# Kernel optimization log

Hardware: AMD Instinct MI355X
Metric: run time of the kernel (lower is better)

The kernel has to match this reference:

```python
import math
import jax, jax.numpy as jnp
import numpy as np

B, N, D, H = 8, 512, 1024, 16
HD = D // H
K_DEFAULT, K_MAX, PROX_THR = 8, 12, 20.0


def setup_inputs() -> dict:
    key = jax.random.key(0)
    ks = jax.random.split(key, 12)
    tokens_B = jax.random.normal(ks[0], (B, N, D), dtype=jnp.float32)
    ego_distances = jax.random.uniform(ks[1], (B, N), dtype=jnp.float32)
    ego_mask = jnp.zeros((B, N), dtype=bool).at[:, 0].set(True)  # token 0 is ego
    ego_speed = jax.random.uniform(ks[2], (B,), dtype=jnp.float32)
    s = 1.0 / math.sqrt(D)
    Wq = jax.random.normal(ks[3], (D, D), jnp.float32) * s
    Wk = jax.random.normal(ks[4], (D, D), jnp.float32) * s
    Wv = jax.random.normal(ks[5], (D, D), jnp.float32) * s
    Weq = jax.random.normal(ks[6], (D, D), jnp.float32) * s
    Wo = jax.random.normal(ks[7], (D, D), jnp.float32) * (0.02 * s)
    Dm = D // 4
    W1 = jax.random.normal(ks[8], (Dm, 2), jnp.float32) * (1.0 / math.sqrt(2))
    b1 = jnp.zeros((Dm,), jnp.float32)
    W2 = jax.random.normal(ks[9], (H, Dm), jnp.float32) * (1.0 / math.sqrt(Dm))
    b2 = jnp.zeros((H,), jnp.float32)
    return dict(tokens_B=tokens_B, ego_distances=ego_distances, ego_mask=ego_mask,
                ego_speed=ego_speed, Wq=Wq, Wk=Wk, Wv=Wv, Weq=Weq, Wo=Wo,
                W1=W1, b1=b1, W2=W2, b2=b2)


def _compute_K(ego_speed, ego_distances):
    # deterministic, no-grad lookup (torch: @torch.no_grad)
    n = ego_distances.shape[1]
    close = (ego_distances < PROX_THR).astype(jnp.float32).sum(-1)
    density = close / max(n, 1)
    avg_speed = float(jnp.mean(ego_speed))
    avg_density = float(jnp.mean(density))
    K = K_DEFAULT
    if avg_speed > 15.0:
        K = min(K + 1, K_MAX)
    if avg_density > 0.5:
        K = min(K + 1, K_MAX)
    return min(K, n - 1)


def reference(tokens_B, ego_distances, ego_mask, ego_speed, Wq, Wk, Wv, Weq, Wo, W1, b1, W2, b2):
    b, n, d = tokens_B.shape
    K = _compute_K(ego_speed, ego_distances)
    if K <= 0:
        return jnp.zeros_like(tokens_B)

    # top-K nearest-to-ego neighbors per token, excluding self
    eye = jnp.eye(n, dtype=bool)
    dist_rank = jnp.where(eye[None, :, :], jnp.inf, ego_distances[:, None, :])  # (B,N,N)
    _, topk_idx = jax.lax.top_k(-dist_rank, K)  # (B,N,K) indices of smallest dists

    neighbors = jax.vmap(lambda t, idx: t[idx])(tokens_B, topk_idx)  # (B,N,K,D)

    is_ego = ego_mask.astype(tokens_B.dtype)[..., None]
    Q = (1.0 - is_ego) * (tokens_B @ Wq.T) + is_ego * (tokens_B @ Weq.T)
    Km = neighbors @ Wk.T
    Vm = neighbors @ Wv.T

    Q = Q.reshape(b, n, H, HD).transpose(0, 2, 1, 3)              # (B,H,N,hd)
    Km = Km.reshape(b, n, K, H, HD).transpose(0, 3, 1, 2, 4)      # (B,H,N,K,hd)
    Vm = Vm.reshape(b, n, K, H, HD).transpose(0, 3, 1, 2, 4)

    scores = jnp.einsum('bhnd,bhnkd->bhnk', Q, Km) / math.sqrt(HD)

    # additive pairwise distance bias MLP on (d_i_to_ego, d_j_to_ego)
    d_i = jnp.broadcast_to(ego_distances[:, :, None], (b, n, K))
    d_j = jax.vmap(lambda dd, idx: dd[idx])(ego_distances, topk_idx)
    dist_pair = jnp.stack([d_i, d_j], axis=-1)                    # (B,N,K,2)
    bias = jax.nn.relu(dist_pair @ W1.T + b1) @ W2.T + b2         # (B,N,K,H)
    scores = scores + bias.transpose(0, 3, 1, 2)                  # FIX-1: additive

    attn = jax.nn.softmax(scores, axis=-1)
    out = jnp.einsum('bhnk,bhnkd->bhnd', attn, Vm)
    out = out.transpose(0, 2, 1, 3).reshape(b, n, d)              # FIX-2 axis order
    return out @ Wo.T
```

## Files before the change

### kernel.cpp

```cpp
#include <hip/hip_runtime.h>
#include <math.h>

#define Bn 8
#define Nn 512
#define Dn 1024
#define Hn 16
#define HDn 64
#define KMAX 12
#define NSMAX 13
#define PROX 20.0f

typedef __attribute__((ext_vector_type(8))) short bf16x8;
typedef __attribute__((ext_vector_type(4))) float f32x4;

__device__ __forceinline__ unsigned short f2bf(float f) {
    unsigned int u = __float_as_uint(f);
    return (unsigned short)((u + 0x7FFFu + ((u >> 16) & 1u)) >> 16);
}

__global__ __launch_bounds__(256) void cvt_meta_kernel(const float* __restrict__ tokens,
                                                       const float* __restrict__ Wq,
                                                       const float* __restrict__ Wo,
                                                       const float* __restrict__ Wk,
                                                       const float* __restrict__ Wv,
                                                       const float* __restrict__ dist,
                                                       const float* __restrict__ speed,
                                                       unsigned short* __restrict__ tok_h,
                                                       unsigned short* __restrict__ wq_h,
                                                       unsigned short* __restrict__ wo_h,
                                                       unsigned short* __restrict__ wkv_h,
                                                       int* __restrict__ meta,
                                                       int* __restrict__ Lidx,
                                                       unsigned short* __restrict__ tok_g) {
    int blk = blockIdx.x;
    if (blk < 8192) {
        const float* src;
        unsigned short* dst;
        int local;
        if (blk < 4096) { src = tokens; dst = tok_h; local = blk; }
        else if (blk < 5120) { src = Wq; dst = wq_h; local = blk - 4096; }
        else if (blk < 6144) { src = Wo; dst = wo_h; local = blk - 5120; }
        else if (blk < 7168) { src = Wk; dst = wkv_h; local = blk - 6144; }
        else { src = Wv; dst = wkv_h + (size_t)Dn * Dn; local = blk - 7168; }
        int i = (local * 256 + threadIdx.x) * 4;
        float4 v = *(const float4*)&src[i];
        ushort4 o;
        o.x = f2bf(v.x); o.y = f2bf(v.y); o.z = f2bf(v.z); o.w = f2bf(v.w);
        *(ushort4*)&dst[i] = o;
        return;
    }
    if (threadIdx.x >= 64) return;
    int lane = threadIdx.x;
    int b = blk - 8192;

    int cnt = 0;
    for (int i = lane; i < Bn * Nn; i += 64) cnt += (dist[i] < PROX) ? 1 : 0;
    for (int off = 32; off; off >>= 1) cnt += __shfl_xor(cnt, off);

    float sp = 0.f;
    for (int i = lane; i < Bn; i += 64) sp += speed[i];
    for (int off = 32; off; off >>= 1) sp += __shfl_xor(sp, off);

    float avg_density = (float)cnt / (float)(Bn * Nn);
    float avg_speed = sp / (float)Bn;
    int K = 8;
    if (avg_speed > 15.0f) K = min(K + 1, KMAX);
    if (avg_density > 0.5f) K = min(K + 1, KMAX);
    K = min(K, Nn - 1);
    if (b == 0 && lane == 0) meta[0] = K;
    int ns = K + 1;

    int sel[NSMAX];
    float dloc[Nn / 64];
    #pragma unroll
    for (int j = 0; j < Nn / 64; ++j) dloc[j] = dist[b * Nn + lane + 64 * j];
    for (int r = 0; r < ns; ++r) {
        float mv = 1e30f;
        int mi = 0;
        #pragma unroll
        for (int j = 0; j < Nn / 64; ++j) {
            if (dloc[j] < mv) { mv = dloc[j]; mi = lane + 64 * j; }
        }
        for (int off = 32; off; off >>= 1) {
            float ov = __shfl_xor(mv, off);
            int oi = __shfl_xor(mi, off);
            if (ov < mv || (ov == mv && oi < mi)) { mv = ov; mi = oi; }
        }
        sel[r] = mi;
        if (lane == 0) Lidx[b * NSMAX + r] = mi;
        if ((mi & 63) == lane) dloc[mi >> 6] = 1e30f;
    }

    for (int s = 0; s < ns; ++s) {
        const float* src = &tokens[(size_t)(b * Nn + sel[s]) * Dn];
        unsigned short* dst = &tok_g[(size_t)(b * 16 + s) * Dn];
        #pragma unroll
        for (int q = 0; q < 4; ++q) {
            float4 v = *(const float4*)&src[(q * 64 + lane) * 4];
            ushort4 o;
            o.x = f2bf(v.x); o.y = f2bf(v.y); o.z = f2bf(v.z); o.w = f2bf(v.w);
            *(ushort4*)&dst[(q * 64 + lane) * 4] = o;
        }
    }
}

__device__ __forceinline__ void gemm_body_s(const unsigned short* A,
                                            const unsigned short* Bm,
                                            float* Cf, unsigned short* Ch,
                                            int Nd, int Kd, int sA, int sB,
                                            int bm, int bn, int mode, int hh,
                                            unsigned short* As, unsigned short* Bs) {
    int t = threadIdx.x;
    int wave = t >> 6, lane = t & 63;
    int wm = wave >> 1, wn = wave & 1;

    int srow = lane >> 2;
    int skoff = (lane & 3) * 8;
    const unsigned short* Ag  = A  + (size_t)(bm + wave * 16 + srow) * sA + skoff;
    const unsigned short* Bg  = Bm + (size_t)(bn + wave * 32 + srow) * sB + skoff;
    const unsigned short* Bg2 = Bg + (size_t)16 * sB;
    unsigned short* AsW  = As + (wave * 16) * 32;
    unsigned short* BsW  = Bs + (wave * 32) * 32;
    unsigned short* BsW2 = BsW + 16 * 32;

    f32x4 acc[2][4] = {};

    int fm = lane & 15;
    int fk = (lane >> 4) * 8;

    for (int k0 = 0; k0 < Kd; k0 += 32) {
        __builtin_amdgcn_global_load_lds((const __attribute__((address_space(1))) void*)Ag,
                                         (__attribute__((address_space(3))) void*)AsW, 16, 0, 0);
        __builtin_amdgcn_global_load_lds((const __attribute__((address_space(1))) void*)Bg,
                                         (__attribute__((address_space(3))) void*)BsW, 16, 0, 0);
        __builtin_amdgcn_global_load_lds((const __attribute__((address_space(1))) void*)Bg2,
                                         (__attribute__((address_space(3))) void*)BsW2, 16, 0, 0);
        Ag += 32; Bg += 32; Bg2 += 32;
        __syncthreads();

        bf16x8 af[2], bfr[4];
        #pragma unroll
        for (int mi = 0; mi < 2; ++mi)
            af[mi] = *(const bf16x8*)&As[(wm * 32 + mi * 16 + fm) * 32 + fk];
        #pragma unroll
        for (int ni = 0; ni < 4; ++ni)
            bfr[ni] = *(const bf16x8*)&Bs[(wn * 64 + ni * 16 + fm) * 32 + fk];
        #pragma unroll
        for (int mi = 0; mi < 2; ++mi)
            #pragma unroll
            for (int ni = 0; ni < 4; ++ni)
                acc[mi][ni] = __builtin_amdgcn_mfma_f32_16x16x32_bf16(af[mi], bfr[ni], acc[mi][ni], 0, 0, 0);
        __syncthreads();
    }

    int erow = (lane >> 4) * 4;
    #pragma unroll
    for (int mi = 0; mi < 2; ++mi)
        #pragma unroll
        for (int ni = 0; ni < 4; ++ni)
            #pragma unroll
            for (int r = 0; r < 4; ++r) {
                int row = bm + wm * 32 + mi * 16 + erow + r;
                int col = bn + wn * 64 + ni * 16 + fm;
                if (mode == 0) {
                    Cf[(size_t)row * Nd + col] = acc[mi][ni][r];
                } else if (mode == 1) {
                    Ch[(size_t)row * Nd + col] = f2bf(acc[mi][ni][r]);
                } else {
                    int bb = col >> 4, ss = col & 15;
                    Ch[((size_t)bb * 1024 + row) * 256 + ss * 16 + hh] = f2bf(acc[mi][ni][r]);
                }
            }
}

__global__ __launch_bounds__(256) void proj_fused_kernel(const unsigned short* __restrict__ tok_h,
                                                         const unsigned short* __restrict__ wq_h,
                                                         const unsigned short* __restrict__ tok_g,
                                                         const unsigned short* __restrict__ wkv_h,
                                                         const float* __restrict__ tokens,
                                                         const float* __restrict__ Weq,
                                                         float* __restrict__ Qbuf,
                                                         float* __restrict__ Kproj,
                                                         unsigned short* __restrict__ v_h,
                                                         float* __restrict__ Qego) {
    __shared__ unsigned short As[64 * 32];
    __shared__ unsigned short Bs[128 * 32];
    __shared__ float tok[Dn];

    int blk = blockIdx.x;
    if (blk < 16) {
        gemm_body_s(tok_g, wkv_h, Kproj, 0, Dn, Dn, Dn, Dn,
                    (blk >> 3) * 64, (blk & 7) * 128, 0, 0, As, Bs);
    } else if (blk < 32) {
        int idx = blk - 16;
        gemm_body_s(tok_g, wkv_h + (size_t)Dn * Dn, 0, v_h, Dn, Dn, Dn, Dn,
                    (idx >> 3) * 64, (idx & 7) * 128, 1, 0, As, Bs);
    } else if (blk < 544) {
        int idx = blk - 32;
        gemm_body_s(tok_h, wq_h, Qbuf, 0, Dn, Dn, Dn, Dn,
                    (idx >> 3) * 64, (idx & 7) * 128, 0, 0, As, Bs);
    } else {
        int blk2 = blk - 544;
        int b = blk2 >> 5, cg = blk2 & 31;
        for (int t = threadIdx.x; t < Dn; t += 256) tok[t] = tokens[(size_t)(b * Nn) * Dn + t];
        __syncthreads();
        int w = threadIdx.x >> 6, lane = threadIdx.x & 63;
        for (int o = 0; o < 8; ++o) {
            int col = cg * 32 + w * 8 + o;
            const float* wr = &Weq[(size_t)col * Dn];
            float sum = 0.f;
            #pragma unroll
            for (int q = 0; q < 4; ++q) {
                float4 w4 = *(const float4*)&wr[q * 256 + lane * 4];
                float4 t4 = *(const float4*)&tok[q * 256 + lane * 4];
                sum += w4.x * t4.x + w4.y * t4.y + w4.z * t4.z + w4.w * t4.w;
            }
            for (int off = 32; off; off >>= 1) sum += __shfl_xor(sum, off);
            if (lane == 0) Qego[(size_t)b * Dn + col] = sum;
        }
    }
}

__global__ __launch_bounds__(256) void vo3_gemm_kernel(const unsigned short* __restrict__ wo_h,
                                                       const unsigned short* __restrict__ v_h,
                                                       unsigned short* __restrict__ Vo3T) {
    __shared__ unsigned short As[64 * 32];
    __shared__ unsigned short Bs[128 * 32];
    int h = blockIdx.y;
    gemm_body_s(wo_h + h * HDn, v_h + h * HDn, 0, Vo3T, 0, HDn, Dn, Dn,
                blockIdx.x * 64, 0, 2, h, As, Bs);
}

#define HSTR 264
__global__ __launch_bounds__(256) void attn_kernel(const float* __restrict__ Q,
                                                   const float* __restrict__ Qego,
                                                   const float* __restrict__ Kproj,
                                                   const float* __restrict__ dist,
                                                   const float* __restrict__ W1,
                                                   const float* __restrict__ b1,
                                                   const float* __restrict__ W2,
                                                   const float* __restrict__ b2,
                                                   const int* __restrict__ meta,
                                                   const int* __restrict__ Lidx,
                                                   unsigned short* __restrict__ Wt) {
    __shared__ float q[Dn];
    __shared__ float hid[KMAX * HSTR];
    __shared__ float sc[Hn * NSMAX];
    __shared__ float at[Hn * NSMAX];
    __shared__ int selslot[NSMAX];
    __shared__ int inv[16];
    __shared__ float dj[NSMAX];

    int bi = blockIdx.x;
    int b = bi >> 9;
    int i = bi & (Nn - 1);
    int K = meta[0];
    int ns = K + 1;
    int t = threadIdx.x;

    if (t == 0) {
        for (int s = 0; s < 16; ++s) inv[s] = -1;
        int cnt = 0;
        for (int s = 0; s < ns && cnt < K; ++s) {
            int jj = Lidx[b * NSMAX + s];
            if (jj != i) { selslot[cnt] = s; dj[cnt] = dist[b * Nn + jj]; inv[s] = cnt; cnt++; }
        }
    }
    {
        const float* qsrc = (i == 0) ? &Qego[(size_t)b * Dn] : &Q[(size_t)bi * Dn];
        float4 v = *(const float4*)&qsrc[t * 4];
        *(float4*)&q[t * 4] = v;
    }
    __syncthreads();

    float d_i = dist[b * Nn + i];

    {
        float2 w01 = *(const float2*)&W1[2 * t];
        float bb = b1[t];
        for (int k = 0; k < K; ++k) {
            float h = w01.x * d_i + w01.y * dj[k] + bb;
            hid[k * HSTR + t] = h > 0.f ? h : 0.f;
        }
    }
    __syncthreads();

    {
        int g = t >> 4, l = t & 15;
        float4 qv = *(const float4*)&q[g * HDn + l * 4];
        float4 w2v[4];
        #pragma unroll
        for (int ii = 0; ii < 4; ++ii)
            w2v[ii] = *(const float4*)&W2[g * 256 + ii * 64 + l * 4];
        float bias0 = b2[g];

        for (int k = 0; k < K; ++k) {
            int row = b * 16 + selslot[k];
            float4 kv4 = *(const float4*)&Kproj[(size_t)row * Dn + g * HDn + l * 4];
            float val = (qv.x * kv4.x + qv.y * kv4.y + qv.z * kv4.z + qv.w * kv4.w) * 0.125f;
            #pragma unroll
            for (int ii = 0; ii < 4; ++ii) {
                float4 h4 = *(const float4*)&hid[k * HSTR + ii * 64 + l * 4];
                val += w2v[ii].x * h4.x + w2v[ii].y * h4.y + w2v[ii].z * h4.z + w2v[ii].w * h4.w;
            }
            val += __shfl_xor(val, 1);
            val += __shfl_xor(val, 2);
            val += __shfl_xor(val, 4);
            val += __shfl_xor(val, 8);
            if (l == 0) sc[g * NSMAX + k] = val + bias0;
        }
    }
    __syncthreads();

    if (t < Hn) {
        int h = t;
        float m = -1e30f;
        for (int k = 0; k < K; ++k) m = fmaxf(m, sc[h * NSMAX + k]);
        float ssum = 0.f;
        for (int k = 0; k < K; ++k) {
            float e = expf(sc[h * NSMAX + k] - m);
            at[h * NSMAX + k] = e;
            ssum += e;
        }
        float inv2 = 1.f / ssum;
        for (int k = 0; k < K; ++k) at[h * NSMAX + k] *= inv2;
    }
    __syncthreads();

    {
        int s = t >> 4, h = t & 15;
        int k = (s < NSMAX) ? inv[s] : -1;
        float a = (k >= 0) ? at[h * NSMAX + k] : 0.f;
        Wt[(size_t)bi * 256 + t] = f2bf(a);
    }
}

__global__ __launch_bounds__(256) void final_gemm_kernel(const unsigned short* __restrict__ Wt,
                                                         const unsigned short* __restrict__ Vo3T,
                                                         float* __restrict__ out) {
    __shared__ unsigned short As[64 * 32];
    __shared__ unsigned short Bs[128 * 32];
    int rbase = blockIdx.y * 64;
    int b = rbase >> 9;
    int bmloc = rbase & (Nn - 1);
    gemm_body_s(Wt + (size_t)b * Nn * 256,
                Vo3T + (size_t)b * Dn * 256,
                out + (size_t)b * Nn * Dn, 0,
                Dn, 256, 256, 256, bmloc, blockIdx.x * 128, 0, 0, As, Bs);
}

extern "C" void kernel_launch(void* const* d_in, const int* in_sizes, int n_in,
                              void* d_out, int out_size, void* d_ws, size_t ws_size,
                              hipStream_t stream) {
    (void)in_sizes; (void)n_in; (void)out_size; (void)ws_size;
    const float* tokens = (const float*)d_in[0];
    const float* dist   = (const float*)d_in[1];
    const float* speed  = (const float*)d_in[3];
    const float* Wq  = (const float*)d_in[4];
    const float* Wk  = (const float*)d_in[5];
    const float* Wv  = (const float*)d_in[6];
    const float* Weq = (const float*)d_in[7];
    const float* Wo  = (const float*)d_in[8];
    const float* W1  = (const float*)d_in[9];
    const float* b1  = (const float*)d_in[10];
    const float* W2  = (const float*)d_in[11];
    const float* b2  = (const float*)d_in[12];
    float* out = (float*)d_out;

    char* ws = (char*)d_ws;
    const size_t SZ_KP   = (size_t)128 * Dn * sizeof(float);
    const size_t SZ_VH   = (size_t)128 * Dn * sizeof(unsigned short);
    const size_t SZ_V3   = (size_t)Bn * Dn * 256 * sizeof(unsigned short);
    const size_t SZ_WT   = (size_t)Bn * Nn * 256 * sizeof(unsigned short);
    const size_t SZ_BIG  = (size_t)Bn * Nn * Dn * sizeof(float);
    const size_t SZ_BIGH = (size_t)Bn * Nn * Dn * sizeof(unsigned short);
    const size_t SZ_WH   = (size_t)Dn * Dn * sizeof(unsigned short);
    const size_t SZ_TG   = (size_t)128 * Dn * sizeof(unsigned short);
    const size_t SZ_QE   = (size_t)Bn * Dn * sizeof(float);

    size_t off = 0;
    int*   meta  = (int*)(ws + off);  off += 256;
    int*   Lidx  = (int*)(ws + off);  off += 768;
    float* Kproj = (float*)(ws + off); off += SZ_KP;
    float* Qbuf  = (float*)(ws + off); off += SZ_BIG;
    float* Qego  = (float*)(ws + off); off += SZ_QE;
    unsigned short* v_h   = (unsigned short*)(ws + off); off += SZ_VH;
    unsigned short* Vo3T  = (unsigned short*)(ws + off); off += SZ_V3;
    unsigned short* Wt    = (unsigned short*)(ws + off); off += SZ_WT;
    unsigned short* tok_h = (unsigned short*)(ws + off); off += SZ_BIGH;
    unsigned short* wq_h  = (unsigned short*)(ws + off); off += SZ_WH;
    unsigned short* wo_h  = (unsigned short*)(ws + off); off += SZ_WH;
    unsigned short* wkv_h = (unsigned short*)(ws + off); off += 2 * SZ_WH;
    unsigned short* tok_g = (unsigned short*)(ws + off); off += SZ_TG;

    cvt_meta_kernel<<<8200, 256, 0, stream>>>(tokens, Wq, Wo, Wk, Wv, dist, speed,
                                              tok_h, wq_h, wo_h, wkv_h, meta, Lidx, tok_g);
    proj_fused_kernel<<<800, 256, 0, stream>>>(tok_h, wq_h, tok_g, wkv_h, tokens, Weq,
                                               Qbuf, Kproj, v_h, Qego);
    vo3_gemm_kernel<<<dim3(16, 16), 256, 0, stream>>>(wo_h, v_h, Vo3T);
    attn_kernel<<<Bn * Nn, 256, 0, stream>>>(Qbuf, Qego, Kproj, dist, W1, b1, W2, b2,
                                             meta, Lidx, Wt);
    final_gemm_kernel<<<dim3(Dn / 128, (Bn * Nn) / 64), 256, 0, stream>>>(Wt, Vo3T, out);
}
```

Measured before the change: 179.4 us.

## Double-buffer GEMM tiles at 128x128 and fuse Vo3 GEMM into attention launch

The shared GEMM body now uses 128x128 output tiles with a 4x4 MFMA accumulator per wave, and double-buffers the LDS stages so the next K-slice loads while the current one computes. Grid sizes for the projection and final GEMMs are reduced to match the larger tiles. The Vo3 GEMM is merged into the attention kernel as extra leading blocks sharing one LDS buffer, which removes a launch and lets the two run side by side. Larger tiles raise register and LDS use and cut block count, which may lower occupancy and parallelism on the small K/V GEMMs. The attention blocks also carry the larger shared allocation.

```diff
diff --git a/kernel.cpp b/kernel.cpp
--- a/kernel.cpp
+++ b/kernel.cpp
@@ -116,51 +116,59 @@
 
     int srow = lane >> 2;
     int skoff = (lane & 3) * 8;
-    const unsigned short* Ag  = A  + (size_t)(bm + wave * 16 + srow) * sA + skoff;
-    const unsigned short* Bg  = Bm + (size_t)(bn + wave * 32 + srow) * sB + skoff;
-    const unsigned short* Bg2 = Bg + (size_t)16 * sB;
-    unsigned short* AsW  = As + (wave * 16) * 32;
-    unsigned short* BsW  = Bs + (wave * 32) * 32;
-    unsigned short* BsW2 = BsW + 16 * 32;
-
-    f32x4 acc[2][4] = {};
-
+    const unsigned short* Ag = A + (size_t)(bm + wave * 32 + srow) * sA + skoff;
+    const unsigned short* Bg = Bm + (size_t)(bn + wave * 32 + srow) * sB + skoff;
+
+    f32x4 acc[4][4] = {};
     int fm = lane & 15;
     int fk = (lane >> 4) * 8;
 
-    for (int k0 = 0; k0 < Kd; k0 += 32) {
+    auto stage = [&](int buf) {
+        unsigned short* dA = As + buf * 4096 + wave * 1024;
+        unsigned short* dB = Bs + buf * 4096 + wave * 1024;
         __builtin_amdgcn_global_load_lds((const __attribute__((address_space(1))) void*)Ag,
-                                         (__attribute__((address_space(3))) void*)AsW, 16, 0, 0);
+                                         (__attribute__((address_space(3))) void*)dA, 16, 0, 0);
+        __builtin_amdgcn_global_load_lds((const __attribute__((address_space(1))) void*)(Ag + (size_t)16 * sA),
+                                         (__attribute__((address_space(3))) void*)(dA + 512), 16, 0, 0);
         __builtin_amdgcn_global_load_lds((const __attribute__((address_space(1))) void*)Bg,
-                                         (__attribute__((address_space(3))) void*)BsW, 16, 0, 0);
-        __builtin_amdgcn_global_load_lds((const __attribute__((address_space(1))) void*)Bg2,
-                                         (__attribute__((address_space(3))) void*)BsW2, 16, 0, 0);
-        Ag += 32; Bg += 32; Bg2 += 32;
-        __syncthreads();
-
-        bf16x8 af[2], bfr[4];
-        #pragma unroll
-        for (int mi = 0; mi < 2; ++mi)
-            af[mi] = *(const bf16x8*)&As[(wm * 32 + mi * 16 + fm) * 32 + fk];
+                                         (__attribute__((address_space(3))) void*)dB, 16, 0, 0);
+        __builtin_amdgcn_global_load_lds((const __attribute__((address_space(1))) void*)(Bg + (size_t)16 * sB),
+                                         (__attribute__((address_space(3))) void*)(dB + 512), 16, 0, 0);
+        Ag += 32; Bg += 32;
+    };
+
+    int nsteps = Kd >> 5;
+    stage(0);
+    __syncthreads();
+    int cur = 0;
+    for (int s = 0; s < nsteps; ++s) {
+        if (s + 1 < nsteps) stage(cur ^ 1);
+        const unsigned short* Ab = As + cur * 4096;
+        const unsigned short* Bb = Bs + cur * 4096;
+        bf16x8 af[4], bfr[4];
+        #pragma unroll
+        for (int mi = 0; mi < 4; ++mi)
+            af[mi] = *(const bf16x8*)&Ab[(wm * 64 + mi * 16 + fm) * 32 + fk];
         #pragma unroll
         for (int ni = 0; ni < 4; ++ni)
-            bfr[ni] = *(const bf16x8*)&Bs[(wn * 64 + ni * 16 + fm) * 32 + fk];
-        #pragma unroll
-        for (int mi = 0; mi < 2; ++mi)
+            bfr[ni] = *(const bf16x8*)&Bb[(wn * 64 + ni * 16 + fm) * 32 + fk];
+        #pragma unroll
+        for (int mi = 0; mi < 4; ++mi)
             #pragma unroll
             for (int ni = 0; ni < 4; ++ni)
                 acc[mi][ni] = __builtin_amdgcn_mfma_f32_16x16x32_bf16(af[mi], bfr[ni], acc[mi][ni], 0, 0, 0);
         __syncthreads();
+        cur ^= 1;
     }
 
     int erow = (lane >> 4) * 4;
     #pragma unroll
-    for (int mi = 0; mi < 2; ++mi)
+    for (int mi = 0; mi < 4; ++mi)
         #pragma unroll
         for (int ni = 0; ni < 4; ++ni)
             #pragma unroll
             for (int r = 0; r < 4; ++r) {
-                int row = bm + wm * 32 + mi * 16 + erow + r;
+                int row = bm + wm * 64 + mi * 16 + erow + r;
                 int col = bn + wn * 64 + ni * 16 + fm;
                 if (mode == 0) {
                     Cf[(size_t)row * Nd + col] = acc[mi][ni][r];
@@ -183,24 +191,24 @@
                                                          float* __restrict__ Kproj,
                                                          unsigned short* __restrict__ v_h,
                                                          float* __restrict__ Qego) {
-    __shared__ unsigned short As[64 * 32];
-    __shared__ unsigned short Bs[128 * 32];
+    __shared__ unsigned short As[2 * 128 * 32];
+    __shared__ unsigned short Bs[2 * 128 * 32];
     __shared__ float tok[Dn];
 
     int blk = blockIdx.x;
-    if (blk < 16) {
+    if (blk < 8) {
         gemm_body_s(tok_g, wkv_h, Kproj, 0, Dn, Dn, Dn, Dn,
-                    (blk >> 3) * 64, (blk & 7) * 128, 0, 0, As, Bs);
-    } else if (blk < 32) {
+                    0, blk * 128, 0, 0, As, Bs);
+    } else if (blk < 16) {
+        int idx = blk - 8;
+        gemm_body_s(tok_g, wkv_h + (size_t)Dn * Dn, 0, v_h, Dn, Dn, Dn, Dn,
+                    0, idx * 128, 1, 0, As, Bs);
+    } else if (blk < 272) {
         int idx = blk - 16;
-        gemm_body_s(tok_g, wkv_h + (size_t)Dn * Dn, 0, v_h, Dn, Dn, Dn, Dn,
-                    (idx >> 3) * 64, (idx & 7) * 128, 1, 0, As, Bs);
-    } else if (blk < 544) {
-        int idx = blk - 32;
         gemm_body_s(tok_h, wq_h, Qbuf, 0, Dn, Dn, Dn, Dn,
-                    (idx >> 3) * 64, (idx & 7) * 128, 0, 0, As, Bs);
+                    (idx >> 3) * 128, (idx & 7) * 128, 0, 0, As, Bs);
     } else {
-        int blk2 = blk - 544;
+        int blk2 = blk - 272;
         int b = blk2 >> 5, cg = blk2 & 31;
         for (int t = threadIdx.x; t < Dn; t += 256) tok[t] = tokens[(size_t)(b * Nn) * Dn + t];
         __syncthreads();
@@ -221,37 +229,41 @@
     }
 }
 
-__global__ __launch_bounds__(256) void vo3_gemm_kernel(const unsigned short* __restrict__ wo_h,
+#define HSTR 264
+__global__ __launch_bounds__(256) void vo3_attn_kernel(const unsigned short* __restrict__ wo_h,
                                                        const unsigned short* __restrict__ v_h,
-                                                       unsigned short* __restrict__ Vo3T) {
-    __shared__ unsigned short As[64 * 32];
-    __shared__ unsigned short Bs[128 * 32];
-    int h = blockIdx.y;
-    gemm_body_s(wo_h + h * HDn, v_h + h * HDn, 0, Vo3T, 0, HDn, Dn, Dn,
-                blockIdx.x * 64, 0, 2, h, As, Bs);
-}
-
-#define HSTR 264
-__global__ __launch_bounds__(256) void attn_kernel(const float* __restrict__ Q,
-                                                   const float* __restrict__ Qego,
-                                                   const float* __restrict__ Kproj,
-                                                   const float* __restrict__ dist,
-                                                   const float* __restrict__ W1,
-                                                   const float* __restrict__ b1,
-                                                   const float* __restrict__ W2,
-                                                   const float* __restrict__ b2,
-                                                   const int* __restrict__ meta,
-                                                   const int* __restrict__ Lidx,
-                                                   unsigned short* __restrict__ Wt) {
-    __shared__ float q[Dn];
-    __shared__ float hid[KMAX * HSTR];
-    __shared__ float sc[Hn * NSMAX];
-    __shared__ float at[Hn * NSMAX];
-    __shared__ int selslot[NSMAX];
-    __shared__ int inv[16];
-    __shared__ float dj[NSMAX];
-
-    int bi = blockIdx.x;
+                                                       unsigned short* __restrict__ Vo3T,
+                                                       const float* __restrict__ Q,
+                                                       const float* __restrict__ Qego,
+                                                       const float* __restrict__ Kproj,
+                                                       const float* __restrict__ dist,
+                                                       const float* __restrict__ W1,
+                                                       const float* __restrict__ b1,
+                                                       const float* __restrict__ W2,
+                                                       const float* __restrict__ b2,
+                                                       const int* __restrict__ meta,
+                                                       const int* __restrict__ Lidx,
+                                                       unsigned short* __restrict__ Wt) {
+    __shared__ __align__(16) char smem[32768];
+
+    int blk = blockIdx.x;
+    if (blk < 128) {
+        int h = blk >> 3;
+        gemm_body_s(wo_h + h * HDn, v_h + h * HDn, 0, Vo3T, 0, HDn, Dn, Dn,
+                    (blk & 7) * 128, 0, 2, h,
+                    (unsigned short*)smem, (unsigned short*)(smem + 16384));
+        return;
+    }
+
+    float* q       = (float*)smem;
+    float* hid     = (float*)(smem + 4096);
+    float* sc      = (float*)(smem + 16768);
+    float* at      = (float*)(smem + 17600);
+    int*   selslot = (int*)(smem + 18432);
+    int*   inv     = (int*)(smem + 18496);
+    float* dj      = (float*)(smem + 18560);
+
+    int bi = blk - 128;
     int b = bi >> 9;
     int i = bi & (Nn - 1);
     int K = meta[0];
@@ -338,9 +350,9 @@
 __global__ __launch_bounds__(256) void final_gemm_kernel(const unsigned short* __restrict__ Wt,
                                                          const unsigned short* __restrict__ Vo3T,
                                                          float* __restrict__ out) {
-    __shared__ unsigned short As[64 * 32];
-    __shared__ unsigned short Bs[128 * 32];
-    int rbase = blockIdx.y * 64;
+    __shared__ unsigned short As[2 * 128 * 32];
+    __shared__ unsigned short Bs[2 * 128 * 32];
+    int rbase = blockIdx.y * 128;
     int b = rbase >> 9;
     int bmloc = rbase & (Nn - 1);
     gemm_body_s(Wt + (size_t)b * Nn * 256,
@@ -395,10 +407,10 @@
 
     cvt_meta_kernel<<<8200, 256, 0, stream>>>(tokens, Wq, Wo, Wk, Wv, dist, speed,
                                               tok_h, wq_h, wo_h, wkv_h, meta, Lidx, tok_g);
-    proj_fused_kernel<<<800, 256, 0, stream>>>(tok_h, wq_h, tok_g, wkv_h, tokens, Weq,
+    proj_fused_kernel<<<528, 256, 0, stream>>>(tok_h, wq_h, tok_g, wkv_h, tokens, Weq,
                                                Qbuf, Kproj, v_h, Qego);
-    vo3_gemm_kernel<<<dim3(16, 16), 256, 0, stream>>>(wo_h, v_h, Vo3T);
-    attn_kernel<<<Bn * Nn, 256, 0, stream>>>(Qbuf, Qego, Kproj, dist, W1, b1, W2, b2,
-                                             meta, Lidx, Wt);
-    final_gemm_kernel<<<dim3(Dn / 128, (Bn * Nn) / 64), 256, 0, stream>>>(Wt, Vo3T, out);
-}
+    vo3_attn_kernel<<<128 + Bn * Nn, 256, 0, stream>>>(wo_h, v_h, Vo3T,
+                                                       Qbuf, Qego, Kproj, dist, W1, b1, W2, b2,
+                                                       meta, Lidx, Wt);
+    final_gemm_kernel<<<dim3(Dn / 128, (Bn * Nn) / 128), 256, 0, stream>>>(Wt, Vo3T, out);
+}
```

After: 203.6 us. 1.13x slower.

## Double-buffer GEMM LDS tiles and parallelize neighbor slot selection with ballot

Applied to the files above, without the earlier changes.

The shared GEMM body now uses two LDS buffers per operand. The next k-slice is issued through global_load_lds while MFMAs run on the current slice, and one barrier per step replaces two. Separately, the serial single-thread neighbor-slot selection in the attention kernel is replaced by a wave-wide ballot and popcount ranking. This doubles the GEMM shared memory footprint, which may reduce occupancy, and it relies on the direct-to-LDS loads completing before the barrier is passed.

```diff
diff --git a/kernel.cpp b/kernel.cpp
--- a/kernel.cpp
+++ b/kernel.cpp
@@ -119,38 +119,45 @@
     const unsigned short* Ag  = A  + (size_t)(bm + wave * 16 + srow) * sA + skoff;
     const unsigned short* Bg  = Bm + (size_t)(bn + wave * 32 + srow) * sB + skoff;
     const unsigned short* Bg2 = Bg + (size_t)16 * sB;
-    unsigned short* AsW  = As + (wave * 16) * 32;
-    unsigned short* BsW  = Bs + (wave * 32) * 32;
-    unsigned short* BsW2 = BsW + 16 * 32;
 
     f32x4 acc[2][4] = {};
-
     int fm = lane & 15;
     int fk = (lane >> 4) * 8;
 
-    for (int k0 = 0; k0 < Kd; k0 += 32) {
+    auto stage = [&](int buf) {
+        unsigned short* AsW  = As + buf * 2048 + (wave * 16) * 32;
+        unsigned short* BsW  = Bs + buf * 4096 + (wave * 32) * 32;
         __builtin_amdgcn_global_load_lds((const __attribute__((address_space(1))) void*)Ag,
                                          (__attribute__((address_space(3))) void*)AsW, 16, 0, 0);
         __builtin_amdgcn_global_load_lds((const __attribute__((address_space(1))) void*)Bg,
                                          (__attribute__((address_space(3))) void*)BsW, 16, 0, 0);
         __builtin_amdgcn_global_load_lds((const __attribute__((address_space(1))) void*)Bg2,
-                                         (__attribute__((address_space(3))) void*)BsW2, 16, 0, 0);
+                                         (__attribute__((address_space(3))) void*)(BsW + 512), 16, 0, 0);
         Ag += 32; Bg += 32; Bg2 += 32;
-        __syncthreads();
-
+    };
+
+    int nsteps = Kd >> 5;
+    stage(0);
+    __syncthreads();
+    int cur = 0;
+    for (int s = 0; s < nsteps; ++s) {
+        if (s + 1 < nsteps) stage(cur ^ 1);
+        const unsigned short* Ab = As + cur * 2048;
+        const unsigned short* Bb = Bs + cur * 4096;
         bf16x8 af[2], bfr[4];
         #pragma unroll
         for (int mi = 0; mi < 2; ++mi)
-            af[mi] = *(const bf16x8*)&As[(wm * 32 + mi * 16 + fm) * 32 + fk];
+            af[mi] = *(const bf16x8*)&Ab[(wm * 32 + mi * 16 + fm) * 32 + fk];
         #pragma unroll
         for (int ni = 0; ni < 4; ++ni)
-            bfr[ni] = *(const bf16x8*)&Bs[(wn * 64 + ni * 16 + fm) * 32 + fk];
+            bfr[ni] = *(const bf16x8*)&Bb[(wn * 64 + ni * 16 + fm) * 32 + fk];
         #pragma unroll
         for (int mi = 0; mi < 2; ++mi)
             #pragma unroll
             for (int ni = 0; ni < 4; ++ni)
                 acc[mi][ni] = __builtin_amdgcn_mfma_f32_16x16x32_bf16(af[mi], bfr[ni], acc[mi][ni], 0, 0, 0);
         __syncthreads();
+        cur ^= 1;
     }
 
     int erow = (lane >> 4) * 4;
@@ -183,8 +190,8 @@
                                                          float* __restrict__ Kproj,
                                                          unsigned short* __restrict__ v_h,
                                                          float* __restrict__ Qego) {
-    __shared__ unsigned short As[64 * 32];
-    __shared__ unsigned short Bs[128 * 32];
+    __shared__ unsigned short As[2 * 64 * 32];
+    __shared__ unsigned short Bs[2 * 128 * 32];
     __shared__ float tok[Dn];
 
     int blk = blockIdx.x;
@@ -224,8 +231,8 @@
 __global__ __launch_bounds__(256) void vo3_gemm_kernel(const unsigned short* __restrict__ wo_h,
                                                        const unsigned short* __restrict__ v_h,
                                                        unsigned short* __restrict__ Vo3T) {
-    __shared__ unsigned short As[64 * 32];
-    __shared__ unsigned short Bs[128 * 32];
+    __shared__ unsigned short As[2 * 64 * 32];
+    __shared__ unsigned short Bs[2 * 128 * 32];
     int h = blockIdx.y;
     gemm_body_s(wo_h + h * HDn, v_h + h * HDn, 0, Vo3T, 0, HDn, Dn, Dn,
                 blockIdx.x * 64, 0, 2, h, As, Bs);
@@ -258,13 +265,20 @@
     int ns = K + 1;
     int t = threadIdx.x;
 
-    if (t == 0) {
-        for (int s = 0; s < 16; ++s) inv[s] = -1;
-        int cnt = 0;
-        for (int s = 0; s < ns && cnt < K; ++s) {
-            int jj = Lidx[b * NSMAX + s];
-            if (jj != i) { selslot[cnt] = s; dj[cnt] = dist[b * Nn + jj]; inv[s] = cnt; cnt++; }
-        }
+    float d_i = dist[b * Nn + i];
+
+    if (t < 64) {
+        int s = t;
+        int jj = (s < ns) ? Lidx[b * NSMAX + s] : -1;
+        bool valid = (s < ns) && (jj != i);
+        unsigned long long mask = __ballot(valid);
+        int rank = __popcll(mask & ((1ull << s) - 1ull));
+        bool take = valid && (rank < K);
+        if (take) {
+            selslot[rank] = s;
+            dj[rank] = dist[b * Nn + jj];
+        }
+        if (s < 16) inv[s] = take ? rank : -1;
     }
     {
         const float* qsrc = (i == 0) ? &Qego[(size_t)b * Dn] : &Q[(size_t)bi * Dn];
@@ -272,8 +286,6 @@
         *(float4*)&q[t * 4] = v;
     }
     __syncthreads();
-
-    float d_i = dist[b * Nn + i];
 
     {
         float2 w01 = *(const float2*)&W1[2 * t];
@@ -338,8 +350,8 @@
 __global__ __launch_bounds__(256) void final_gemm_kernel(const unsigned short* __restrict__ Wt,
                                                          const unsigned short* __restrict__ Vo3T,
                                                          float* __restrict__ out) {
-    __shared__ unsigned short As[64 * 32];
-    __shared__ unsigned short Bs[128 * 32];
+    __shared__ unsigned short As[2 * 64 * 32];
+    __shared__ unsigned short Bs[2 * 128 * 32];
     int rbase = blockIdx.y * 64;
     int b = rbase >> 9;
     int bmloc = rbase & (Nn - 1);
```

Measured after the change: 179.3 us. About the same (-0.1%).
